# Performance work log

Hardware: AMD Instinct MI355X
Metric: run time of the kernel (lower is better)

The kernel has to match this reference:

```python
import jax, jax.numpy as jnp
import numpy as np

N, C, NS, S = 32768, 128, 16, 8  # points, channels (mid==out planes), nsample, share_planes
EPS = 1e-5


def setup_inputs() -> dict:
    rng = np.random.default_rng(0)
    p = (rng.standard_normal((N, 3)) * 2.0).astype(np.float32)
    # exact kNN indices (self included), chunked to bound memory -- int constants
    sq = (p * p).sum(1)
    idx = np.empty((N, NS), dtype=np.int32)
    CH = 4096
    for i in range(0, N, CH):
        d = sq[i:i + CH, None] + sq[None, :] - 2.0 * (p[i:i + CH] @ p.T)
        idx[i:i + CH] = np.argpartition(d, NS, axis=1)[:, :NS]

    def lin(fi, fo):
        return (rng.standard_normal((fi, fo)).astype(np.float32) / np.sqrt(fi),
                np.zeros((fo,), np.float32))

    Wq, bq = lin(C, C)
    Wk, bk = lin(C, C)
    Wv, bv = lin(C, C)
    pW1, pb1 = lin(3, 3)
    pW2, pb2 = lin(3, C)
    wW1, wb1 = lin(C, C // S)
    wW2, wb2 = lin(C // S, C // S)
    x = rng.standard_normal((N, C)).astype(np.float32)
    d = dict(p=p, x=x,
             Wq=Wq, bq=bq, Wk=Wk, bk=bk, Wv=Wv, bv=bv,
             pW1=pW1, pb1=pb1, pg1=np.ones(3, np.float32), pbe1=np.zeros(3, np.float32),
             pW2=pW2, pb2=pb2,
             wg1=np.ones(C, np.float32), wbe1=np.zeros(C, np.float32),
             wW1=wW1, wb1=wb1,
             wg2=np.ones(C // S, np.float32), wbe2=np.zeros(C // S, np.float32),
             wW2=wW2, wb2=wb2,
             idx=idx)
    return {k: jnp.asarray(v) for k, v in d.items()}


def _bn(t, g, b):
    # BatchNorm1d training-mode over [N, nsample, ch]: stats per channel over N*nsample
    mu = t.mean(axis=(0, 1), keepdims=True)
    var = t.var(axis=(0, 1), keepdims=True)
    return (t - mu) * jax.lax.rsqrt(var + EPS) * g + b


def reference(p, x, Wq, bq, Wk, bk, Wv, bv, pW1, pb1, pg1, pbe1, pW2, pb2,
              wg1, wbe1, wW1, wb1, wg2, wbe2, wW2, wb2, idx):
    xq = x @ Wq + bq                      # [N, C]
    xk = (x @ Wk + bk)[idx]               # kNN gather -> [N, NS, C]
    xv = (x @ Wv + bv)[idx]               # [N, NS, C]
    pr = p[idx] - p[:, None, :]           # relative positions [N, NS, 3]
    # linear_p: Linear(3,3) -> BN(3) -> ReLU -> Linear(3,C)
    pr = jax.nn.relu(_bn(pr @ pW1 + pb1, pg1, pbe1)) @ pW2 + pb2  # [N, NS, C]
    # subtraction vector attention; out_planes//mid_planes == 1 so p_r sum(2) == p_r
    w = xk - xq[:, None, :] + pr
    # linear_w: BN(C) -> ReLU -> Linear(C, C//S) -> BN(C//S) -> ReLU -> Linear(C//S, C//S)
    w = jax.nn.relu(_bn(w, wg1, wbe1)) @ wW1 + wb1
    w = jax.nn.relu(_bn(w, wg2, wbe2)) @ wW2 + wb2                # [N, NS, C//S]
    w = jax.nn.softmax(w, axis=1)                                 # softmax over neighbors
    # share_planes-grouped weighted aggregate
    out = ((xv + pr).reshape(N, NS, S, C // S) * w[:, :, None, :]).sum(1).reshape(N, C)
    return out
```

## Files before the change

### kernel.cpp

```cpp
#include <hip/hip_runtime.h>

typedef unsigned short u16;
#define DEV __device__ __forceinline__

typedef short bf16x8 __attribute__((ext_vector_type(8)));
typedef float f32x4  __attribute__((ext_vector_type(4)));

constexpr int NP = 32768;
constexpr int C  = 128;
constexpr int NS = 16;
constexpr int RTOT = NP * NS;
constexpr float EPS = 1e-5f;
constexpr float INV_R = 1.0f / (float)RTOT;

constexpr size_t oXQ = 0;
constexpr size_t oXK = (size_t)NP * C * 2;
constexpr size_t oXV = oXK * 2;
constexpr size_t oW1 = oXK * 3;
constexpr size_t oPA = oW1;
constexpr size_t oPB = oW1 + 16384;
constexpr size_t oST = oW1 + (size_t)RTOT * 16 * 2;
constexpr size_t oM1 = oST;
constexpr size_t oM2 = oM1 + 16*8*4;
constexpr size_t oM3 = oM2 + 16*256*4;
constexpr size_t oPC = oM3 + 16*32*4;
constexpr size_t oWT = oPC + 256*32*4;
constexpr size_t WS_NEED = oWT + 3*128*128*2;

DEV float bu2f(u16 v){ return __uint_as_float(((unsigned)v) << 16); }
DEV u16 f2bu(float f){
  unsigned u = __float_as_uint(f);
  return (u16)((u + 0x7fffu + ((u >> 16) & 1u)) >> 16);
}
DEV unsigned pk2(float a, float b){ return (unsigned)f2bu(a) | ((unsigned)f2bu(b) << 16); }
DEV unsigned pk2tr(float a, float b){
  return (__float_as_uint(a) >> 16) | (__float_as_uint(b) & 0xffff0000u);
}
DEV void b2x2(unsigned v, float& lo, float& hi){
  lo = __uint_as_float(v << 16);
  hi = __uint_as_float(v & 0xffff0000u);
}
DEV int clampg(int g){ return g < 0 ? 0 : (g > NP-1 ? NP-1 : g); }

__global__ __launch_bounds__(256) void k_sig(float* __restrict__ out, float val){
  int i = blockIdx.x * 256 + threadIdx.x;
  if (i < NP*C) out[i] = val;
}

__global__ __launch_bounds__(256) void k_finA(const float* __restrict__ part,
                                              float* __restrict__ mid,
                                              int slots, int width){
  __shared__ float red[4][64];
  const int l = threadIdx.x & 63, w = threadIdx.x >> 6;
  const int ch = blockIdx.x * 64 + l;
  const int y = blockIdx.y;
  const int cs = slots >> 4;
  const int n4 = cs >> 2;
  float a0 = 0.f, a1 = 0.f, a2 = 0.f, a3 = 0.f;
  if (ch < width){
    const float* base = part + (size_t)(y*cs + w*n4) * width + ch;
    int j = 0;
    for (; j + 4 <= n4; j += 4){
      a0 += base[(size_t)(j  ) * width];
      a1 += base[(size_t)(j+1) * width];
      a2 += base[(size_t)(j+2) * width];
      a3 += base[(size_t)(j+3) * width];
    }
    for (; j < n4; ++j) a0 += base[(size_t)j * width];
  }
  red[w][l] = (a0 + a1) + (a2 + a3);
  __syncthreads();
  if (threadIdx.x < 64 && ch < width)
    mid[(size_t)y * width + ch] = red[0][l] + red[1][l] + red[2][l] + red[3][l];
}

__global__ __launch_bounds__(256) void k_wt(const float* __restrict__ Wq,
                                            const float* __restrict__ Wk,
                                            const float* __restrict__ Wv,
                                            u16* __restrict__ wt){
  const int mat = blockIdx.y;
  const float* W = (mat==0) ? Wq : ((mat==1) ? Wk : Wv);
  int e = blockIdx.x * 256 + threadIdx.x;
  int k = e >> 7, c = e & 127;
  wt[mat*16384 + c*128 + k] = f2bu(W[e]);
}

__global__ __launch_bounds__(256) void k_qkv(const float* __restrict__ x,
                                             const u16* __restrict__ wt,
                                             const float* __restrict__ bq,
                                             const float* __restrict__ bk,
                                             const float* __restrict__ bv,
                                             u16* __restrict__ outw){
  __shared__ __align__(16) u16 xb[64*136];
  __shared__ __align__(16) u16 wtl[128*136];
  const int t = threadIdx.x;
  const int row0 = blockIdx.x * 64;
  {
    const float4* xs = (const float4*)(x + (size_t)row0 * C);
    #pragma unroll
    for (int i = 0; i < 8; ++i){
      int chunk = t + i*256;
      int row = chunk >> 5;
      int cp  = (chunk & 31) * 4;
      float4 v = xs[chunk];
      *(uint2*)&xb[row*136 + cp] = make_uint2(pk2(v.x, v.y), pk2(v.z, v.w));
    }
  }
  __syncthreads();
  const int w = t >> 6, l = t & 63;
  const int quad = l >> 4, col = l & 15;
  bf16x8 afrag[4];
  {
    const u16* abase = &xb[(size_t)(w*16 + col) * 136];
    #pragma unroll
    for (int kk = 0; kk < 4; ++kk)
      afrag[kk] = *(const bf16x8*)(abase + kk*32 + quad*8);
  }
  for (int mat = 0; mat < 3; ++mat){
    const float* bias = (mat==0) ? bq : ((mat==1) ? bk : bv);
    {
      const uint4* ws4 = (const uint4*)(wt + mat*16384);
      #pragma unroll
      for (int i = 0; i < 8; ++i){
        int chunk = t + i*256;
        int c = chunk >> 4, kp = (chunk & 15) * 8;
        *(uint4*)&wtl[c*136 + kp] = ws4[chunk];
      }
    }
    __syncthreads();
    u16* outp = outw + (size_t)mat * NP * C + (size_t)(row0 + w*16) * C;
    #pragma unroll
    for (int ct = 0; ct < 8; ++ct){
      bf16x8 bfrag[4];
      const u16* bbase = &wtl[(size_t)(ct*16 + col) * 136];
      #pragma unroll
      for (int kk = 0; kk < 4; ++kk)
        bfrag[kk] = *(const bf16x8*)(bbase + kk*32 + quad*8);
      float bv0 = bias[ct*16 + col];
      f32x4 acc; acc[0] = bv0; acc[1] = bv0; acc[2] = bv0; acc[3] = bv0;
      #pragma unroll
      for (int kk = 0; kk < 4; ++kk)
        acc = __builtin_amdgcn_mfma_f32_16x16x32_bf16(afrag[kk], bfrag[kk], acc, 0, 0, 0);
      #pragma unroll
      for (int i = 0; i < 4; ++i)
        outp[(size_t)(quad*4 + i) * C + ct*16 + col] = f2bu(acc[i]);
    }
    __syncthreads();
  }
}

__global__ __launch_bounds__(256) void k_bn1(const float* __restrict__ p,
                                             const int* __restrict__ idx,
                                             const float* __restrict__ pW1,
                                             const float* __restrict__ pb1,
                                             float* __restrict__ partials1){
  __shared__ float wred[4][8];
  const int t = threadIdx.x;
  float w[9], b3[3];
  #pragma unroll
  for (int i = 0; i < 9; ++i) w[i] = pW1[i];
  #pragma unroll
  for (int i = 0; i < 3; ++i) b3[i] = pb1[i];
  float s[3] = {0,0,0}, q[3] = {0,0,0};
  const int base = blockIdx.x * 1024 + t;
  #pragma unroll
  for (int i = 0; i < 4; ++i){
    int r = base + i*256;
    int g = clampg(idx[r]);
    int n = r >> 4;
    float d0 = p[3*g]   - p[3*n];
    float d1 = p[3*g+1] - p[3*n+1];
    float d2 = p[3*g+2] - p[3*n+2];
    #pragma unroll
    for (int k = 0; k < 3; ++k){
      float tv = d0*w[k] + d1*w[3+k] + d2*w[6+k] + b3[k];
      s[k] += tv; q[k] = fmaf(tv, tv, q[k]);
    }
  }
  #pragma unroll
  for (int k = 0; k < 3; ++k){
    #pragma unroll
    for (int m = 1; m < 64; m <<= 1){
      s[k] += __shfl_xor(s[k], m);
      q[k] += __shfl_xor(q[k], m);
    }
  }
  if ((t & 63) == 0){
    int wv = t >> 6;
    wred[wv][0] = s[0]; wred[wv][1] = s[1]; wred[wv][2] = s[2]; wred[wv][3] = 0.f;
    wred[wv][4] = q[0]; wred[wv][5] = q[1]; wred[wv][6] = q[2]; wred[wv][7] = 0.f;
  }
  __syncthreads();
  if (t < 8)
    partials1[blockIdx.x*8 + t] = wred[0][t] + wred[1][t] + wred[2][t] + wred[3][t];
}

__global__ __launch_bounds__(256) void k_bn2(const float* __restrict__ p,
                                             const int* __restrict__ idx,
                                             const float* __restrict__ pW1,
                                             const float* __restrict__ pb1,
                                             const float* __restrict__ pg1,
                                             const float* __restrict__ pbe1,
                                             const float* __restrict__ pW2,
                                             const float* __restrict__ pb2,
                                             const u16* __restrict__ xq,
                                             const u16* __restrict__ xk,
                                             const float* __restrict__ mid1,
                                             float* __restrict__ partials2){
  __shared__ float sq0[64], sq1[64], sq2[64];
  __shared__ int   sgi[64];
  __shared__ __align__(16) float4 pW2t[128];
  __shared__ float bn1s[8];
  __shared__ __align__(16) float redS[4][128], redQ[4][128];
  const int t = threadIdx.x;
  if (t < 3){
    float sv = 0.f, sq = 0.f;
    for (int i = 0; i < 16; ++i){ sv += mid1[i*8+t]; sq += mid1[i*8+4+t]; }
    float mu = sv * INV_R, var = sq * INV_R - mu*mu;
    float rs = rsqrtf(var + EPS);
    float sc = rs * pg1[t];
    bn1s[t]   = sc;
    bn1s[4+t] = pb1[t] * sc + pbe1[t] - mu * sc;
  }
  if (t < 128)
    pW2t[t] = make_float4(pW2[t], pW2[128+t], pW2[256+t], pb2[t]);
  float w9[9];
  if (t < 64){
    #pragma unroll
    for (int i = 0; i < 9; ++i) w9[i] = pW1[i];
  }
  __syncthreads();
  const int w = t >> 6, l = t & 63;
  const float4 pwA = pW2t[2*l], pwB = pW2t[2*l+1];
  float sA = 0.f, qA = 0.f, sB = 0.f, qB = 0.f;

  for (int tile = 0; tile < 4; ++tile){
    const int b0 = (blockIdx.x * 4 + tile) * 64;
    if (t < 64){
      int r = b0 + t, n = r >> 4;
      int g = clampg(idx[r]);
      float d0 = p[3*g]   - p[3*n];
      float d1 = p[3*g+1] - p[3*n+1];
      float d2 = p[3*g+2] - p[3*n+2];
      sq0[t] = fmaxf((d0*w9[0] + d1*w9[3] + d2*w9[6]) * bn1s[0] + bn1s[4], 0.f);
      sq1[t] = fmaxf((d0*w9[1] + d1*w9[4] + d2*w9[7]) * bn1s[1] + bn1s[5], 0.f);
      sq2[t] = fmaxf((d0*w9[2] + d1*w9[5] + d2*w9[8]) * bn1s[2] + bn1s[6], 0.f);
      sgi[t] = g;
    }
    __syncthreads();
    #pragma unroll
    for (int pt = 0; pt < 4; ++pt){
      const int n = (b0 >> 4) + pt;
      unsigned qx = *(const unsigned*)(xq + (size_t)n*C + 2*l);
      float xqA, xqB; b2x2(qx, xqA, xqB);
      #pragma unroll
      for (int k = 0; k < 4; ++k){
        int rr = pt*16 + w + k*4;
        int g = sgi[rr];
        unsigned kx = *(const unsigned*)(xk + (size_t)g*C + 2*l);
        float xkA, xkB; b2x2(kx, xkA, xkB);
        float prA = sq0[rr]*pwA.x + sq1[rr]*pwA.y + sq2[rr]*pwA.z + pwA.w;
        float prB = sq0[rr]*pwB.x + sq1[rr]*pwB.y + sq2[rr]*pwB.z + pwB.w;
        float w0A = xkA - xqA + prA;
        float w0B = xkB - xqB + prB;
        sA += w0A; qA = fmaf(w0A, w0A, qA);
        sB += w0B; qB = fmaf(w0B, w0B, qB);
      }
    }
    __syncthreads();
  }
  *(float2*)&redS[w][2*l] = make_float2(sA, sB);
  *(float2*)&redQ[w][2*l] = make_float2(qA, qB);
  __syncthreads();
  if (t < 128){
    partials2[(size_t)blockIdx.x*256 + t]       = redS[0][t]+redS[1][t]+redS[2][t]+redS[3][t];
    partials2[(size_t)blockIdx.x*256 + 128 + t] = redQ[0][t]+redQ[1][t]+redQ[2][t]+redQ[3][t];
  }
}

__global__ __launch_bounds__(256) void k_w1(const float* __restrict__ p,
                                            const int* __restrict__ idx,
                                            const float* __restrict__ pW1,
                                            const float* __restrict__ pb1,
                                            const float* __restrict__ pg1,
                                            const float* __restrict__ pbe1,
                                            const float* __restrict__ pW2,
                                            const float* __restrict__ pb2,
                                            const float* __restrict__ wg1,
                                            const float* __restrict__ wbe1,
                                            const float* __restrict__ wW1,
                                            const float* __restrict__ wb1,
                                            const u16* __restrict__ xq,
                                            const u16* __restrict__ xk,
                                            u16* __restrict__ w1out,
                                            const float* __restrict__ mid1,
                                            const float* __restrict__ mid2){
  __shared__ __align__(16) float4 pW2t[128];
  __shared__ float2 ss2[128];
  __shared__ float bn1s[8];
  __shared__ float wb1f[16];
  __shared__ float pW1f[9];
  __shared__ float sq0[64], sq1[64], sq2[64];
  __shared__ int   sgi[64];
  __shared__ __align__(16) u16 hsb[64*136];
  const int t = threadIdx.x;
  if (t < 3){
    float sv = 0.f, sq = 0.f;
    for (int i = 0; i < 16; ++i){ sv += mid1[i*8+t]; sq += mid1[i*8+4+t]; }
    float mu = sv * INV_R, var = sq * INV_R - mu*mu;
    float rs = rsqrtf(var + EPS);
    float sc = rs * pg1[t];
    bn1s[t]   = sc;
    bn1s[4+t] = pb1[t] * sc + pbe1[t] - mu * sc;
  }
  if (t < 9)  pW1f[t] = pW1[t];
  if (t < 16) wb1f[t] = wb1[t];
  if (t < 128){
    pW2t[t] = make_float4(pW2[t], pW2[128+t], pW2[256+t], pb2[t]);
    float sv = 0.f, sq = 0.f;
    for (int i = 0; i < 16; ++i){ sv += mid2[i*256+t]; sq += mid2[i*256+128+t]; }
    float mu = sv * INV_R, var = sq * INV_R - mu*mu;
    float rs = rsqrtf(var + EPS);
    float sc = rs * wg1[t];
    ss2[t] = make_float2(sc, wbe1[t] - mu * sc);
  }

  const int w = t >> 6, l = t & 63;
  const int quad = l >> 4, col = l & 15;
  bf16x8 bfrag[4];
  #pragma unroll
  for (int kk = 0; kk < 4; ++kk){
    #pragma unroll
    for (int j = 0; j < 8; ++j)
      bfrag[kk][j] = (short)f2bu(wW1[(size_t)(kk*32 + quad*8 + j)*16 + col]);
  }
  __syncthreads();

  const float4 pwA = pW2t[2*l], pwB = pW2t[2*l+1];
  const float2 scA = ss2[2*l],  scB = ss2[2*l+1];
  const float biasC = wb1f[col];

  for (int tile = 0; tile < 4; ++tile){
    const int rb = (blockIdx.x * 4 + tile) * 64;
    if (t < 64){
      int r = rb + t, n = r >> 4;
      int g = clampg(idx[r]);
      float d0 = p[3*g]   - p[3*n];
      float d1 = p[3*g+1] - p[3*n+1];
      float d2 = p[3*g+2] - p[3*n+2];
      sq0[t] = fmaxf((d0*pW1f[0] + d1*pW1f[3] + d2*pW1f[6]) * bn1s[0] + bn1s[4], 0.f);
      sq1[t] = fmaxf((d0*pW1f[1] + d1*pW1f[4] + d2*pW1f[7]) * bn1s[1] + bn1s[5], 0.f);
      sq2[t] = fmaxf((d0*pW1f[2] + d1*pW1f[5] + d2*pW1f[8]) * bn1s[2] + bn1s[6], 0.f);
      sgi[t] = g;
    }
    __syncthreads();
    #pragma unroll
    for (int pt = 0; pt < 4; ++pt){
      const int n = (rb >> 4) + pt;
      unsigned qx = *(const unsigned*)(xq + (size_t)n*C + 2*l);
      float xqA, xqB; b2x2(qx, xqA, xqB);
      #pragma unroll
      for (int k = 0; k < 4; ++k){
        int rr = pt*16 + w + k*4;
        int g = sgi[rr];
        unsigned kx = *(const unsigned*)(xk + (size_t)g*C + 2*l);
        float xkA, xkB; b2x2(kx, xkA, xkB);
        float prA = sq0[rr]*pwA.x + sq1[rr]*pwA.y + sq2[rr]*pwA.z + pwA.w;
        float prB = sq0[rr]*pwB.x + sq1[rr]*pwB.y + sq2[rr]*pwB.z + pwB.w;
        float hA = fmaxf(fmaf(xkA - xqA + prA, scA.x, scA.y), 0.f);
        float hB = fmaxf(fmaf(xkB - xqB + prB, scB.x, scB.y), 0.f);
        *(unsigned*)&hsb[rr*136 + 2*l] = pk2tr(hA, hB);
      }
    }
    __syncthreads();
    f32x4 acc;
    acc[0] = biasC; acc[1] = biasC; acc[2] = biasC; acc[3] = biasC;
    const u16* hbase = &hsb[(size_t)(w*16 + col) * 136];
    #pragma unroll
    for (int kk = 0; kk < 4; ++kk){
      bf16x8 af = *(const bf16x8*)(hbase + kk*32 + quad*8);
      acc = __builtin_amdgcn_mfma_f32_16x16x32_bf16(af, bfrag[kk], acc, 0, 0, 0);
    }
    #pragma unroll
    for (int i = 0; i < 4; ++i){
      int row = w*16 + quad*4 + i;
      w1out[(size_t)(rb + row) * 16 + col] = f2bu(acc[i]);
    }
    __syncthreads();
  }
}

__global__ __launch_bounds__(256) void k_bn3(const u16* __restrict__ w1ws,
                                             float* __restrict__ partials3){
  __shared__ float rs[256][8], rq[256][8];
  const int t = threadIdx.x;
  float s[8], q[8];
  #pragma unroll
  for (int k = 0; k < 8; ++k){ s[k] = 0.f; q[k] = 0.f; }
  const uint4* w4 = (const uint4*)w1ws;
  const int base = blockIdx.x * 256 + t;
  #pragma unroll 4
  for (int it = 0; it < 16; ++it){
    uint4 v = w4[base + it * 65536];
    #pragma unroll
    for (int k = 0; k < 4; ++k){
      float lo, hi; b2x2((&v.x)[k], lo, hi);
      s[k*2]   += lo; q[k*2]   = fmaf(lo, lo, q[k*2]);
      s[k*2+1] += hi; q[k*2+1] = fmaf(hi, hi, q[k*2+1]);
    }
  }
  #pragma unroll
  for (int k = 0; k < 8; ++k){ rs[t][k] = s[k]; rq[t][k] = q[k]; }
  __syncthreads();
  if (t < 32){
    int isq = t >> 4, ch = t & 15;
    int par = ch >> 3, k = ch & 7;
    float acc = 0.f;
    if (isq){
      for (int i2 = par; i2 < 256; i2 += 2) acc += rq[i2][k];
    } else {
      for (int i2 = par; i2 < 256; i2 += 2) acc += rs[i2][k];
    }
    partials3[blockIdx.x*32 + isq*16 + ch] = acc;
  }
}

__global__ __launch_bounds__(256) void k_out(const float* __restrict__ p,
                                             const int* __restrict__ idx,
                                             const float* __restrict__ pW1,
                                             const float* __restrict__ pb1,
                                             const float* __restrict__ pg1,
                                             const float* __restrict__ pbe1,
                                             const float* __restrict__ pW2,
                                             const float* __restrict__ pb2,
                                             const float* __restrict__ wg2,
                                             const float* __restrict__ wbe2,
                                             const float* __restrict__ wW2,
                                             const float* __restrict__ wb2,
                                             const u16* __restrict__ xv,
                                             const u16* __restrict__ w1ws,
                                             const float* __restrict__ mid1,
                                             const float* __restrict__ mid3,
                                             float* __restrict__ out){
  __shared__ __align__(16) float4 pW2t[128];
  __shared__ float pW1f[9];
  __shared__ float bn1s[8];
  __shared__ float sc3[16], sh3[16], wb2f[16];
  __shared__ float wW2f[256];
  __shared__ float s_w2[16*16*16];
  __shared__ float s_q0[256], s_q1[256], s_q2[256];
  __shared__ int   s_g[256];
  const int t = threadIdx.x;
  if (t < 3){
    float sv = 0.f, sq = 0.f;
    for (int i = 0; i < 16; ++i){ sv += mid1[i*8+t]; sq += mid1[i*8+4+t]; }
    float mu = sv * INV_R, var = sq * INV_R - mu*mu;
    float rs = rsqrtf(var + EPS);
    float sc = rs * pg1[t];
    bn1s[t]   = sc;
    bn1s[4+t] = pb1[t] * sc + pbe1[t] - mu * sc;
  }
  if (t < 9) pW1f[t] = pW1[t];
  if (t < 16){
    float sv = 0.f, sq = 0.f;
    for (int i = 0; i < 16; ++i){ sv += mid3[i*32+t]; sq += mid3[i*32+16+t]; }
    float mu = sv * INV_R, var = sq * INV_R - mu*mu;
    float rs = rsqrtf(var + EPS);
    float sc = rs * wg2[t];
    sc3[t] = sc;
    sh3[t] = wbe2[t] - mu * sc;
    wb2f[t] = wb2[t];
  }
  if (t < 128)
    pW2t[t] = make_float4(pW2[t], pW2[128+t], pW2[256+t], pb2[t]);
  wW2f[t] = wW2[t];
  __syncthreads();

  const int pt = t >> 4;
  const int jj = t & 15;
  const int n0 = blockIdx.x * 16;
  {
    const int n = n0 + pt;
    const int r = n * NS + jj;
    const int g = clampg(idx[r]);
    float d0 = p[3*g]   - p[3*n];
    float d1 = p[3*g+1] - p[3*n+1];
    float d2 = p[3*g+2] - p[3*n+2];
    s_q0[t] = fmaxf((d0*pW1f[0] + d1*pW1f[3] + d2*pW1f[6]) * bn1s[0] + bn1s[4], 0.f);
    s_q1[t] = fmaxf((d0*pW1f[1] + d1*pW1f[4] + d2*pW1f[7]) * bn1s[1] + bn1s[5], 0.f);
    s_q2[t] = fmaxf((d0*pW1f[2] + d1*pW1f[5] + d2*pW1f[8]) * bn1s[2] + bn1s[6], 0.f);
    s_g[t]  = g;
    const uint4* wp = (const uint4*)(w1ws + (size_t)r * 16);
    uint4 Wa = wp[0], Wb = wp[1];
    float h2[16];
    #pragma unroll
    for (int o2 = 0; o2 < 4; ++o2){
      float lo, hi;
      b2x2((&Wa.x)[o2], lo, hi);
      h2[o2*2]     = fmaxf(lo * sc3[o2*2]     + sh3[o2*2],     0.f);
      h2[o2*2+1]   = fmaxf(hi * sc3[o2*2+1]   + sh3[o2*2+1],   0.f);
      b2x2((&Wb.x)[o2], lo, hi);
      h2[8+o2*2]   = fmaxf(lo * sc3[8+o2*2]   + sh3[8+o2*2],   0.f);
      h2[8+o2*2+1] = fmaxf(hi * sc3[8+o2*2+1] + sh3[8+o2*2+1], 0.f);
    }
    float w2[16];
    #pragma unroll
    for (int o = 0; o < 16; ++o) w2[o] = wb2f[o];
    #pragma unroll
    for (int o2 = 0; o2 < 16; ++o2){
      float h = h2[o2];
      const float* wr = &wW2f[o2*16];
      #pragma unroll
      for (int o = 0; o < 16; ++o) w2[o] = fmaf(h, wr[o], w2[o]);
    }
    float* dst = &s_w2[(pt*16 + jj)*16];
    #pragma unroll
    for (int o = 0; o < 16; ++o) dst[o] = w2[o];
  }
  __syncthreads();
  const int cs = t & 15;
  {
    float mx = -1e30f;
    #pragma unroll
    for (int j2 = 0; j2 < 16; ++j2) mx = fmaxf(mx, s_w2[(pt*16+j2)*16 + cs]);
    float e[16]; float sum = 0.f;
    #pragma unroll
    for (int j2 = 0; j2 < 16; ++j2){
      e[j2] = __expf(s_w2[(pt*16+j2)*16 + cs] - mx);
      sum += e[j2];
    }
    float inv = 1.0f / sum;
    #pragma unroll
    for (int j2 = 0; j2 < 16; ++j2) s_w2[(pt*16+j2)*16 + cs] = e[j2] * inv;
  }
  __syncthreads();
  const int w = t >> 6, l = t & 63;
  const float4 pwA = pW2t[2*l], pwB = pW2t[2*l+1];
  const int csA = (2*l) & 15;
  #pragma unroll
  for (int pp = 0; pp < 4; ++pp){
    const int pt2 = pp * 4 + w;
    const int n = n0 + pt2;
    float accA = 0.f, accB = 0.f;
    #pragma unroll
    for (int j = 0; j < 16; ++j){
      const int base = pt2*16 + j;
      float2 pj2 = *(const float2*)&s_w2[base*16 + csA];
      int g = s_g[base];
      float qa = s_q0[base], qb = s_q1[base], qc = s_q2[base];
      unsigned v = *(const unsigned*)(xv + (size_t)g*C + 2*l);
      float xvA, xvB; b2x2(v, xvA, xvB);
      float prA = qa*pwA.x + qb*pwA.y + qc*pwA.z + pwA.w;
      float prB = qa*pwB.x + qb*pwB.y + qc*pwB.z + pwB.w;
      accA = fmaf(xvA + prA, pj2.x, accA);
      accB = fmaf(xvB + prB, pj2.y, accB);
    }
    *(float2*)(out + (size_t)n*C + 2*l) = make_float2(accA, accB);
  }
}

extern "C" void kernel_launch(void* const* d_in, const int* in_sizes, int n_in,
                              void* d_out, int out_size, void* d_ws, size_t ws_size,
                              hipStream_t stream) {
  bool ok = (n_in == 23) && (out_size == NP*C) &&
            in_sizes[0] == NP*3 && in_sizes[1] == NP*C &&
            in_sizes[2] == C*C  && in_sizes[8] == 9 &&
            in_sizes[12] == 3*C && in_sizes[16] == C*(C/8) &&
            in_sizes[20] == (C/8)*(C/8) && in_sizes[22] == RTOT;
  if (!ok){
    k_sig<<<(NP*C+255)/256, 256, 0, stream>>>((float*)d_out, 10000.0f);
    return;
  }
  if (ws_size < WS_NEED){
    k_sig<<<(NP*C+255)/256, 256, 0, stream>>>((float*)d_out, 20000.0f);
    return;
  }
  const float* p    = (const float*)d_in[0];
  const float* x    = (const float*)d_in[1];
  const float* Wq   = (const float*)d_in[2];
  const float* bq   = (const float*)d_in[3];
  const float* Wk   = (const float*)d_in[4];
  const float* bk   = (const float*)d_in[5];
  const float* Wv   = (const float*)d_in[6];
  const float* bv   = (const float*)d_in[7];
  const float* pW1  = (const float*)d_in[8];
  const float* pb1  = (const float*)d_in[9];
  const float* pg1  = (const float*)d_in[10];
  const float* pbe1 = (const float*)d_in[11];
  const float* pW2  = (const float*)d_in[12];
  const float* pb2  = (const float*)d_in[13];
  const float* wg1  = (const float*)d_in[14];
  const float* wbe1 = (const float*)d_in[15];
  const float* wW1  = (const float*)d_in[16];
  const float* wb1  = (const float*)d_in[17];
  const float* wg2  = (const float*)d_in[18];
  const float* wbe2 = (const float*)d_in[19];
  const float* wW2  = (const float*)d_in[20];
  const float* wb2  = (const float*)d_in[21];
  const int* idx    = (const int*)d_in[22];

  char* ws = (char*)d_ws;
  u16* xq    = (u16*)(ws + oXQ);
  u16* xk    = (u16*)(ws + oXK);
  u16* xv    = (u16*)(ws + oXV);
  u16* w1ws  = (u16*)(ws + oW1);
  float* pa  = (float*)(ws + oPA);
  float* pb  = (float*)(ws + oPB);
  float* pc  = (float*)(ws + oPC);
  float* m1  = (float*)(ws + oM1);
  float* m2  = (float*)(ws + oM2);
  float* m3  = (float*)(ws + oM3);
  u16* wtp   = (u16*)(ws + oWT);

  k_wt <<<dim3(64, 3), 256, 0, stream>>>(Wq, Wk, Wv, wtp);
  k_qkv<<<512, 256, 0, stream>>>(x, wtp, bq, bk, bv, xq);
  k_bn1<<<512, 256, 0, stream>>>(p, idx, pW1, pb1, pa);
  k_finA<<<dim3(1, 16), 256, 0, stream>>>(pa, m1, 512, 8);
  k_bn2<<<2048, 256, 0, stream>>>(p, idx, pW1, pb1, pg1, pbe1, pW2, pb2,
                                  xq, xk, m1, pb);
  k_finA<<<dim3(4, 16), 256, 0, stream>>>(pb, m2, 2048, 256);
  k_w1 <<<2048, 256, 0, stream>>>(p, idx, pW1, pb1, pg1, pbe1, pW2, pb2,
                                  wg1, wbe1, wW1, wb1, xq, xk, w1ws, m1, m2);
  k_bn3<<<256, 256, 0, stream>>>(w1ws, pc);
  k_finA<<<dim3(1, 16), 256, 0, stream>>>(pc, m3, 256, 32);
  k_out<<<2048, 256, 0, stream>>>(p, idx, pW1, pb1, pg1, pbe1, pW2, pb2,
                                  wg2, wbe2, wW2, wb2, xv, w1ws, m1, m3,
                                  (float*)d_out);
}
```

Before: 231.7 us.

## Fuse third BN statistics into k_w1 epilogue and restructure per-point neighbor loops

Drops the separate k_bn3 kernel. k_w1 now accumulates per-channel sum and sum-of-squares straight from the MFMA fp32 accumulators, so the bf16 intermediate no longer has to be read back. In k_bn2 and k_w1, all 256 threads now precompute the geometry for the whole block's rows in one pass, and each wave then handles whole points across their 16 neighbors, which removes the per-tile barriers. The workspace layout is moved so the partial buffers no longer alias the w1 buffer. One side effect is that the statistics now come from unrounded fp32 values rather than the stored bf16, which changes the numerics slightly.

New measurement: 220.5 us. 4.8% less time.

```diff
diff --git a/kernel.cpp b/kernel.cpp
--- a/kernel.cpp
+++ b/kernel.cpp
@@ -17,14 +17,13 @@
 constexpr size_t oXK = (size_t)NP * C * 2;
 constexpr size_t oXV = oXK * 2;
 constexpr size_t oW1 = oXK * 3;
-constexpr size_t oPA = oW1;
-constexpr size_t oPB = oW1 + 16384;
-constexpr size_t oST = oW1 + (size_t)RTOT * 16 * 2;
-constexpr size_t oM1 = oST;
+constexpr size_t oPA = oW1 + (size_t)RTOT * 16 * 2;
+constexpr size_t oPB = oPA + 512*8*4;
+constexpr size_t oPC = oPB + (size_t)2048*256*4;
+constexpr size_t oM1 = oPC + (size_t)2048*32*4;
 constexpr size_t oM2 = oM1 + 16*8*4;
 constexpr size_t oM3 = oM2 + 16*256*4;
-constexpr size_t oPC = oM3 + 16*32*4;
-constexpr size_t oWT = oPC + 256*32*4;
+constexpr size_t oWT = oM3 + 16*32*4;
 constexpr size_t WS_NEED = oWT + 3*128*128*2;
 
 DEV float bu2f(u16 v){ return __uint_as_float(((unsigned)v) << 16); }
@@ -207,8 +206,8 @@
                                              const u16* __restrict__ xk,
                                              const float* __restrict__ mid1,
                                              float* __restrict__ partials2){
-  __shared__ float sq0[64], sq1[64], sq2[64];
-  __shared__ int   sgi[64];
+  __shared__ float sq0[256], sq1[256], sq2[256];
+  __shared__ int   sgi[256];
   __shared__ __align__(16) float4 pW2t[128];
   __shared__ float bn1s[8];
   __shared__ __align__(16) float redS[4][128], redQ[4][128];
@@ -225,49 +224,43 @@
   if (t < 128)
     pW2t[t] = make_float4(pW2[t], pW2[128+t], pW2[256+t], pb2[t]);
   float w9[9];
-  if (t < 64){
-    #pragma unroll
-    for (int i = 0; i < 9; ++i) w9[i] = pW1[i];
+  #pragma unroll
+  for (int i = 0; i < 9; ++i) w9[i] = pW1[i];
+  __syncthreads();
+  {
+    int r = blockIdx.x * 256 + t, n = r >> 4;
+    int g = clampg(idx[r]);
+    float d0 = p[3*g]   - p[3*n];
+    float d1 = p[3*g+1] - p[3*n+1];
+    float d2 = p[3*g+2] - p[3*n+2];
+    sq0[t] = fmaxf((d0*w9[0] + d1*w9[3] + d2*w9[6]) * bn1s[0] + bn1s[4], 0.f);
+    sq1[t] = fmaxf((d0*w9[1] + d1*w9[4] + d2*w9[7]) * bn1s[1] + bn1s[5], 0.f);
+    sq2[t] = fmaxf((d0*w9[2] + d1*w9[5] + d2*w9[8]) * bn1s[2] + bn1s[6], 0.f);
+    sgi[t] = g;
   }
   __syncthreads();
   const int w = t >> 6, l = t & 63;
   const float4 pwA = pW2t[2*l], pwB = pW2t[2*l+1];
   float sA = 0.f, qA = 0.f, sB = 0.f, qB = 0.f;
-
-  for (int tile = 0; tile < 4; ++tile){
-    const int b0 = (blockIdx.x * 4 + tile) * 64;
-    if (t < 64){
-      int r = b0 + t, n = r >> 4;
-      int g = clampg(idx[r]);
-      float d0 = p[3*g]   - p[3*n];
-      float d1 = p[3*g+1] - p[3*n+1];
-      float d2 = p[3*g+2] - p[3*n+2];
-      sq0[t] = fmaxf((d0*w9[0] + d1*w9[3] + d2*w9[6]) * bn1s[0] + bn1s[4], 0.f);
-      sq1[t] = fmaxf((d0*w9[1] + d1*w9[4] + d2*w9[7]) * bn1s[1] + bn1s[5], 0.f);
-      sq2[t] = fmaxf((d0*w9[2] + d1*w9[5] + d2*w9[8]) * bn1s[2] + bn1s[6], 0.f);
-      sgi[t] = g;
-    }
-    __syncthreads();
-    #pragma unroll
-    for (int pt = 0; pt < 4; ++pt){
-      const int n = (b0 >> 4) + pt;
-      unsigned qx = *(const unsigned*)(xq + (size_t)n*C + 2*l);
-      float xqA, xqB; b2x2(qx, xqA, xqB);
-      #pragma unroll
-      for (int k = 0; k < 4; ++k){
-        int rr = pt*16 + w + k*4;
-        int g = sgi[rr];
-        unsigned kx = *(const unsigned*)(xk + (size_t)g*C + 2*l);
-        float xkA, xkB; b2x2(kx, xkA, xkB);
-        float prA = sq0[rr]*pwA.x + sq1[rr]*pwA.y + sq2[rr]*pwA.z + pwA.w;
-        float prB = sq0[rr]*pwB.x + sq1[rr]*pwB.y + sq2[rr]*pwB.z + pwB.w;
-        float w0A = xkA - xqA + prA;
-        float w0B = xkB - xqB + prB;
-        sA += w0A; qA = fmaf(w0A, w0A, qA);
-        sB += w0B; qB = fmaf(w0B, w0B, qB);
-      }
-    }
-    __syncthreads();
+  #pragma unroll
+  for (int pp = 0; pp < 4; ++pp){
+    const int nl = w*4 + pp;
+    const int n  = blockIdx.x*16 + nl;
+    unsigned qx = *(const unsigned*)(xq + (size_t)n*C + 2*l);
+    float xqA, xqB; b2x2(qx, xqA, xqB);
+    #pragma unroll
+    for (int j = 0; j < 16; ++j){
+      int rr = nl*16 + j;
+      int g = sgi[rr];
+      unsigned kx = *(const unsigned*)(xk + (size_t)g*C + 2*l);
+      float xkA, xkB; b2x2(kx, xkA, xkB);
+      float prA = sq0[rr]*pwA.x + sq1[rr]*pwA.y + sq2[rr]*pwA.z + pwA.w;
+      float prB = sq0[rr]*pwB.x + sq1[rr]*pwB.y + sq2[rr]*pwB.z + pwB.w;
+      float w0A = xkA - xqA + prA;
+      float w0B = xkB - xqB + prB;
+      sA += w0A; qA = fmaf(w0A, w0A, qA);
+      sB += w0B; qB = fmaf(w0B, w0B, qB);
+    }
   }
   *(float2*)&redS[w][2*l] = make_float2(sA, sB);
   *(float2*)&redQ[w][2*l] = make_float2(qA, qB);
@@ -294,15 +287,17 @@
                                             const u16* __restrict__ xk,
                                             u16* __restrict__ w1out,
                                             const float* __restrict__ mid1,
-                                            const float* __restrict__ mid2){
+                                            const float* __restrict__ mid2,
+                                            float* __restrict__ pc){
   __shared__ __align__(16) float4 pW2t[128];
   __shared__ float2 ss2[128];
   __shared__ float bn1s[8];
   __shared__ float wb1f[16];
   __shared__ float pW1f[9];
-  __shared__ float sq0[64], sq1[64], sq2[64];
-  __shared__ int   sgi[64];
+  __shared__ float sq0[256], sq1[256], sq2[256];
+  __shared__ int   sgi[256];
   __shared__ __align__(16) u16 hsb[64*136];
+  __shared__ float wredS[4][16], wredQ[4][16];
   const int t = threadIdx.x;
   if (t < 3){
     float sv = 0.f, sq = 0.f;
@@ -324,7 +319,6 @@
     float sc = rs * wg1[t];
     ss2[t] = make_float2(sc, wbe1[t] - mu * sc);
   }
-
   const int w = t >> 6, l = t & 63;
   const int quad = l >> 4, col = l & 15;
   bf16x8 bfrag[4];
@@ -335,41 +329,41 @@
       bfrag[kk][j] = (short)f2bu(wW1[(size_t)(kk*32 + quad*8 + j)*16 + col]);
   }
   __syncthreads();
+  {
+    int r = blockIdx.x * 256 + t, n = r >> 4;
+    int g = clampg(idx[r]);
+    float d0 = p[3*g]   - p[3*n];
+    float d1 = p[3*g+1] - p[3*n+1];
+    float d2 = p[3*g+2] - p[3*n+2];
+    sq0[t] = fmaxf((d0*pW1f[0] + d1*pW1f[3] + d2*pW1f[6]) * bn1s[0] + bn1s[4], 0.f);
+    sq1[t] = fmaxf((d0*pW1f[1] + d1*pW1f[4] + d2*pW1f[7]) * bn1s[1] + bn1s[5], 0.f);
+    sq2[t] = fmaxf((d0*pW1f[2] + d1*pW1f[5] + d2*pW1f[8]) * bn1s[2] + bn1s[6], 0.f);
+    sgi[t] = g;
+  }
+  __syncthreads();
 
   const float4 pwA = pW2t[2*l], pwB = pW2t[2*l+1];
   const float2 scA = ss2[2*l],  scB = ss2[2*l+1];
   const float biasC = wb1f[col];
+  float sSt = 0.f, qSt = 0.f;
 
   for (int tile = 0; tile < 4; ++tile){
-    const int rb = (blockIdx.x * 4 + tile) * 64;
-    if (t < 64){
-      int r = rb + t, n = r >> 4;
-      int g = clampg(idx[r]);
-      float d0 = p[3*g]   - p[3*n];
-      float d1 = p[3*g+1] - p[3*n+1];
-      float d2 = p[3*g+2] - p[3*n+2];
-      sq0[t] = fmaxf((d0*pW1f[0] + d1*pW1f[3] + d2*pW1f[6]) * bn1s[0] + bn1s[4], 0.f);
-      sq1[t] = fmaxf((d0*pW1f[1] + d1*pW1f[4] + d2*pW1f[7]) * bn1s[1] + bn1s[5], 0.f);
-      sq2[t] = fmaxf((d0*pW1f[2] + d1*pW1f[5] + d2*pW1f[8]) * bn1s[2] + bn1s[6], 0.f);
-      sgi[t] = g;
-    }
-    __syncthreads();
-    #pragma unroll
-    for (int pt = 0; pt < 4; ++pt){
-      const int n = (rb >> 4) + pt;
+    {
+      const int nl = tile*4 + w;
+      const int n  = blockIdx.x*16 + nl;
       unsigned qx = *(const unsigned*)(xq + (size_t)n*C + 2*l);
       float xqA, xqB; b2x2(qx, xqA, xqB);
       #pragma unroll
-      for (int k = 0; k < 4; ++k){
-        int rr = pt*16 + w + k*4;
-        int g = sgi[rr];
+      for (int j = 0; j < 16; ++j){
+        int rrb = nl*16 + j;
+        int g = sgi[rrb];
         unsigned kx = *(const unsigned*)(xk + (size_t)g*C + 2*l);
         float xkA, xkB; b2x2(kx, xkA, xkB);
-        float prA = sq0[rr]*pwA.x + sq1[rr]*pwA.y + sq2[rr]*pwA.z + pwA.w;
-        float prB = sq0[rr]*pwB.x + sq1[rr]*pwB.y + sq2[rr]*pwB.z + pwB.w;
+        float prA = sq0[rrb]*pwA.x + sq1[rrb]*pwA.y + sq2[rrb]*pwA.z + pwA.w;
+        float prB = sq0[rrb]*pwB.x + sq1[rrb]*pwB.y + sq2[rrb]*pwB.z + pwB.w;
         float hA = fmaxf(fmaf(xkA - xqA + prA, scA.x, scA.y), 0.f);
         float hB = fmaxf(fmaf(xkB - xqB + prB, scB.x, scB.y), 0.f);
-        *(unsigned*)&hsb[rr*136 + 2*l] = pk2tr(hA, hB);
+        *(unsigned*)&hsb[(w*16 + j)*136 + 2*l] = pk2tr(hA, hB);
       }
     }
     __syncthreads();
@@ -381,47 +375,24 @@
       bf16x8 af = *(const bf16x8*)(hbase + kk*32 + quad*8);
       acc = __builtin_amdgcn_mfma_f32_16x16x32_bf16(af, bfrag[kk], acc, 0, 0, 0);
     }
+    const int rowbase = blockIdx.x*256 + tile*64 + w*16 + quad*4;
     #pragma unroll
     for (int i = 0; i < 4; ++i){
-      int row = w*16 + quad*4 + i;
-      w1out[(size_t)(rb + row) * 16 + col] = f2bu(acc[i]);
+      w1out[(size_t)(rowbase + i) * 16 + col] = f2bu(acc[i]);
+      sSt += acc[i];
+      qSt = fmaf(acc[i], acc[i], qSt);
     }
     __syncthreads();
   }
-}
-
-__global__ __launch_bounds__(256) void k_bn3(const u16* __restrict__ w1ws,
-                                             float* __restrict__ partials3){
-  __shared__ float rs[256][8], rq[256][8];
-  const int t = threadIdx.x;
-  float s[8], q[8];
-  #pragma unroll
-  for (int k = 0; k < 8; ++k){ s[k] = 0.f; q[k] = 0.f; }
-  const uint4* w4 = (const uint4*)w1ws;
-  const int base = blockIdx.x * 256 + t;
-  #pragma unroll 4
-  for (int it = 0; it < 16; ++it){
-    uint4 v = w4[base + it * 65536];
-    #pragma unroll
-    for (int k = 0; k < 4; ++k){
-      float lo, hi; b2x2((&v.x)[k], lo, hi);
-      s[k*2]   += lo; q[k*2]   = fmaf(lo, lo, q[k*2]);
-      s[k*2+1] += hi; q[k*2+1] = fmaf(hi, hi, q[k*2+1]);
-    }
-  }
-  #pragma unroll
-  for (int k = 0; k < 8; ++k){ rs[t][k] = s[k]; rq[t][k] = q[k]; }
-  __syncthreads();
-  if (t < 32){
-    int isq = t >> 4, ch = t & 15;
-    int par = ch >> 3, k = ch & 7;
-    float acc = 0.f;
-    if (isq){
-      for (int i2 = par; i2 < 256; i2 += 2) acc += rq[i2][k];
-    } else {
-      for (int i2 = par; i2 < 256; i2 += 2) acc += rs[i2][k];
-    }
-    partials3[blockIdx.x*32 + isq*16 + ch] = acc;
+  sSt += __shfl_xor(sSt, 16); sSt += __shfl_xor(sSt, 32);
+  qSt += __shfl_xor(qSt, 16); qSt += __shfl_xor(qSt, 32);
+  if (l < 16){ wredS[w][l] = sSt; wredQ[w][l] = qSt; }
+  __syncthreads();
+  if (t < 16)
+    pc[(size_t)blockIdx.x*32 + t] = wredS[0][t]+wredS[1][t]+wredS[2][t]+wredS[3][t];
+  else if (t < 32){
+    int c = t - 16;
+    pc[(size_t)blockIdx.x*32 + 16 + c] = wredQ[0][c]+wredQ[1][c]+wredQ[2][c]+wredQ[3][c];
   }
 }
 
@@ -620,9 +591,8 @@
                                   xq, xk, m1, pb);
   k_finA<<<dim3(4, 16), 256, 0, stream>>>(pb, m2, 2048, 256);
   k_w1 <<<2048, 256, 0, stream>>>(p, idx, pW1, pb1, pg1, pbe1, pW2, pb2,
-                                  wg1, wbe1, wW1, wb1, xq, xk, w1ws, m1, m2);
-  k_bn3<<<256, 256, 0, stream>>>(w1ws, pc);
-  k_finA<<<dim3(1, 16), 256, 0, stream>>>(pc, m3, 256, 32);
+                                  wg1, wbe1, wW1, wb1, xq, xk, w1ws, m1, m2, pc);
+  k_finA<<<dim3(1, 16), 256, 0, stream>>>(pc, m3, 2048, 32);
   k_out<<<2048, 256, 0, stream>>>(p, idx, pW1, pb1, pg1, pbe1, pW2, pb2,
                                   wg2, wbe2, wW2, wb2, xv, w1ws, m1, m3,
                                   (float*)d_out);
```
